# Performance work log

Measured on AMD Instinct MI355X. Metric: run time of the kernel, lower is better.

Reference implementation:

```python
import jax, jax.numpy as jnp
import numpy as np

B, D, U = 4096, 2048, 2048

def setup_inputs() -> dict:
    key = jax.random.key(0)
    ks = jax.random.split(key, 16)
    s_in = 1.0 / np.sqrt(D)
    s_h = 1.0 / np.sqrt(U)
    inp = {
        "x": jax.random.normal(ks[0], (B, D), jnp.float32),
        "h": jax.random.normal(ks[1], (B, U), jnp.float32),
        "c": jax.random.normal(ks[2], (B, U), jnp.float32),
        # input-to-gate weights (Dense with bias)
        "Wxf": jax.random.normal(ks[3], (D, U), jnp.float32) * s_in,
        "Wxi": jax.random.normal(ks[4], (D, U), jnp.float32) * s_in,
        "Wxo": jax.random.normal(ks[5], (D, U), jnp.float32) * s_in,
        "Wxg": jax.random.normal(ks[6], (D, U), jnp.float32) * s_in,
        "bf": jnp.zeros((U,), jnp.float32),
        "bi": jnp.zeros((U,), jnp.float32),
        "bo": jnp.zeros((U,), jnp.float32),
        "bg": jnp.zeros((U,), jnp.float32),
        # hidden-to-gate weights (no bias)
        "Whf": jax.random.normal(ks[7], (U, U), jnp.float32) * s_h,
        "Whi": jax.random.normal(ks[8], (U, U), jnp.float32) * s_h,
        "Who": jax.random.normal(ks[9], (U, U), jnp.float32) * s_h,
        "Whg": jax.random.normal(ks[10], (U, U), jnp.float32) * s_h,
    }
    return inp

def reference(x, h, c, Wxf, Wxi, Wxo, Wxg, bf, bi, bo, bg, Whf, Whi, Who, Whg):
    # Fuse the 8 small GEMMs into two batched GEMMs over concatenated weights,
    # then one elementwise gate-fusion pass. Math identical to per-Dense form.
    Wx = jnp.concatenate([Wxf, Wxi, Wxo, Wxg], axis=1)   # [D, 4U]
    Wh = jnp.concatenate([Whf, Whi, Who, Whg], axis=1)   # [U, 4U]
    b = jnp.concatenate([bf, bi, bo, bg], axis=0)        # [4U]
    z = x @ Wx + h @ Wh + b                               # [B, 4U]
    zf, zi, zo, zg = jnp.split(z, 4, axis=1)
    f = jax.nn.sigmoid(zf)
    i = jax.nn.sigmoid(zi)
    o = jax.nn.sigmoid(zo)
    g = jnp.tanh(zg)
    c_new = f * c + i * g
    h_new = o * jnp.tanh(c_new)
    return (h_new, c_new)
```

## Files before the change

### kernel.cpp

```cpp
#include <hip/hip_runtime.h>
#include <hip/hip_bf16.h>
#include <stdint.h>

#define B_ 4096
#define D_ 2048
#define U_ 2048
#define K_ 4096
#define N_ 8192

typedef __bf16 bf16x8 __attribute__((ext_vector_type(8)));
typedef float floatx4 __attribute__((ext_vector_type(4)));
typedef unsigned short ushort8 __attribute__((ext_vector_type(8)));

__device__ __forceinline__ unsigned short f2bf(float f) {
    union { float f; unsigned int u; } v; v.f = f;
    unsigned int u = v.u;
    unsigned int r = (u + 0x7fffu + ((u >> 16) & 1u)) >> 16;
    return (unsigned short)r;
}

__device__ __forceinline__ float bf2f(unsigned short b) {
    union { unsigned int u; float f; } v;
    v.u = ((unsigned int)b) << 16;
    return v.f;
}

__device__ __forceinline__ float sigmoid_(float x) {
    return 1.0f / (1.0f + __expf(-x));
}
__device__ __forceinline__ float tanh_(float x) {
    return 1.0f - 2.0f / (__expf(2.0f * x) + 1.0f);
}

__global__ void k_convA(const float* __restrict__ x, const float* __restrict__ h,
                        unsigned short* __restrict__ Abf) {
    int t = blockIdx.x * blockDim.x + threadIdx.x;
    long e = (long)t * 4;
    int b = (int)(e >> 12);
    int k = (int)(e & 4095);
    const float* src = (k < D_) ? (x + (size_t)b * D_ + k)
                                : (h + (size_t)b * U_ + (k - D_));
    float4 v = *(const float4*)src;
    ushort4 o;
    o.x = f2bf(v.x); o.y = f2bf(v.y); o.z = f2bf(v.z); o.w = f2bf(v.w);
    *(ushort4*)(Abf + e) = o;
}

__global__ __launch_bounds__(256) void k_convB(
        const float* __restrict__ Wx0, const float* __restrict__ Wx1,
        const float* __restrict__ Wx2, const float* __restrict__ Wx3,
        const float* __restrict__ Wh0, const float* __restrict__ Wh1,
        const float* __restrict__ Wh2, const float* __restrict__ Wh3,
        unsigned short* __restrict__ Bt) {
    __shared__ float tile[64][65];
    const int g  = blockIdx.z;
    const int k0 = blockIdx.x * 64;
    const int u0 = blockIdx.y * 64;
    const int t  = threadIdx.x;
    const float* W;
    if (k0 < D_) {
        W = (g == 0 ? Wx0 : g == 1 ? Wx1 : g == 2 ? Wx2 : Wx3) + (size_t)k0 * U_;
    } else {
        W = (g == 0 ? Wh0 : g == 1 ? Wh1 : g == 2 ? Wh2 : Wh3) + (size_t)(k0 - D_) * U_;
    }
    {
        const int kr_b = t >> 4;
        const int uc   = (t & 15) * 4;
        #pragma unroll
        for (int p = 0; p < 4; ++p) {
            int kr = p * 16 + kr_b;
            float4 v = *(const float4*)(W + (size_t)kr * U_ + u0 + uc);
            tile[kr][uc + 0] = v.x;
            tile[kr][uc + 1] = v.y;
            tile[kr][uc + 2] = v.z;
            tile[kr][uc + 3] = v.w;
        }
    }
    __syncthreads();
    {
        const int kc = (t & 7) * 8;
        #pragma unroll
        for (int p = 0; p < 2; ++p) {
            int u_idx = p * 32 + (t >> 3);
            int u = u0 + u_idx;
            int nrow = g * U_ + u;
            ushort8 o;
            #pragma unroll
            for (int kk = 0; kk < 8; ++kk)
                o[kk] = f2bf(tile[kc + kk][u_idx]);
            *(ushort8*)(Bt + (size_t)nrow * K_ + k0 + kc) = o;
        }
    }
}

__device__ __forceinline__ void gload16(const unsigned short* g, unsigned short* l) {
    __builtin_amdgcn_global_load_lds(
        (const __attribute__((address_space(1))) void*)g,
        (__attribute__((address_space(3))) void*)l, 16, 0, 0);
}

__global__ __launch_bounds__(256) void k_gemm(const unsigned short* __restrict__ A,
                                              const unsigned short* __restrict__ Bt,
                                              unsigned short* __restrict__ Z) {
    const int id    = blockIdx.x;
    const int xcd   = id & 7;
    const int s     = id >> 3;
    const int m_blk = (xcd << 2) | (s & 3);
    const int n_blk = s >> 2;
    const int m0 = m_blk * 128;
    const int n0 = n_blk * 128;

    __shared__ __align__(16) unsigned short As[2][128 * 32];
    __shared__ __align__(16) unsigned short Bs[2][128 * 32];
    const int tid = threadIdx.x;
    const int w   = tid >> 6;
    const int l   = tid & 63;

    const unsigned short* gA = A  + (size_t)(m0 + w * 16 + (l >> 2)) * K_ + (l & 3) * 8;
    const unsigned short* gB = Bt + (size_t)(n0 + w * 16 + (l >> 2)) * K_ + (l & 3) * 8;
    unsigned short* lA0 = As[0] + w * 512;
    unsigned short* lA1 = As[1] + w * 512;
    unsigned short* lB0 = Bs[0] + w * 512;
    unsigned short* lB1 = Bs[1] + w * 512;

    const int r     = l & 15;
    const int quad  = l >> 4;
    const int m_off = (w & 1) * 64;
    const int n_off = (w >> 1) * 64;

    floatx4 acc[4][4];
    #pragma unroll
    for (int i = 0; i < 4; ++i)
        #pragma unroll
        for (int j = 0; j < 4; ++j)
            #pragma unroll
            for (int e = 0; e < 4; ++e) acc[i][j][e] = 0.f;

    for (int k0 = 0; k0 < K_; k0 += 64) {
        __syncthreads();
        gload16(gA + k0,                        lA0);
        gload16(gA + k0 + (size_t)64 * K_,      lA0 + 2048);
        gload16(gB + k0,                        lB0);
        gload16(gB + k0 + (size_t)64 * K_,      lB0 + 2048);
        gload16(gA + k0 + 32,                   lA1);
        gload16(gA + k0 + 32 + (size_t)64 * K_, lA1 + 2048);
        gload16(gB + k0 + 32,                   lB1);
        gload16(gB + k0 + 32 + (size_t)64 * K_, lB1 + 2048);
        __syncthreads();

        #pragma unroll
        for (int p = 0; p < 2; ++p) {
            bf16x8 af[4], bfv[4];
            #pragma unroll
            for (int i = 0; i < 4; ++i)
                af[i] = *(const bf16x8*)(As[p] + ((m_off + i * 16 + r) * 32 + quad * 8));
            #pragma unroll
            for (int j = 0; j < 4; ++j)
                bfv[j] = *(const bf16x8*)(Bs[p] + ((n_off + j * 16 + r) * 32 + quad * 8));
            #pragma unroll
            for (int i = 0; i < 4; ++i)
                #pragma unroll
                for (int j = 0; j < 4; ++j)
                    acc[i][j] = __builtin_amdgcn_mfma_f32_16x16x32_bf16(
                        af[i], bfv[j], acc[i][j], 0, 0, 0);
        }
    }

    #pragma unroll
    for (int i = 0; i < 4; ++i) {
        #pragma unroll
        for (int j = 0; j < 4; ++j) {
            int col = n0 + n_off + j * 16 + r;
            #pragma unroll
            for (int e = 0; e < 4; ++e) {
                int row = m0 + m_off + i * 16 + quad * 4 + e;
                Z[(size_t)row * N_ + col] = f2bf(acc[i][j][e]);
            }
        }
    }
}

__global__ void k_gates(const unsigned short* __restrict__ Z, const float* __restrict__ c,
                        const float* __restrict__ bfp, const float* __restrict__ bip,
                        const float* __restrict__ bop, const float* __restrict__ bgp,
                        float* __restrict__ hout, float* __restrict__ cout) {
    int t = blockIdx.x * blockDim.x + threadIdx.x;
    long e = (long)t * 4;
    int b = (int)(e >> 11);
    int u = (int)(e & 2047);
    const size_t zr = (size_t)b * N_;
    ushort4 zf4 = *(const ushort4*)(Z + zr + u);
    ushort4 zi4 = *(const ushort4*)(Z + zr + U_ + u);
    ushort4 zo4 = *(const ushort4*)(Z + zr + 2 * U_ + u);
    ushort4 zg4 = *(const ushort4*)(Z + zr + 3 * U_ + u);
    float4 bfv = *(const float4*)(bfp + u);
    float4 biv = *(const float4*)(bip + u);
    float4 bov = *(const float4*)(bop + u);
    float4 bgv = *(const float4*)(bgp + u);
    float4 cv  = *(const float4*)(c + e);

    float zf[4] = {bf2f(zf4.x), bf2f(zf4.y), bf2f(zf4.z), bf2f(zf4.w)};
    float zi[4] = {bf2f(zi4.x), bf2f(zi4.y), bf2f(zi4.z), bf2f(zi4.w)};
    float zo[4] = {bf2f(zo4.x), bf2f(zo4.y), bf2f(zo4.z), bf2f(zo4.w)};
    float zg[4] = {bf2f(zg4.x), bf2f(zg4.y), bf2f(zg4.z), bf2f(zg4.w)};
    float bff[4] = {bfv.x, bfv.y, bfv.z, bfv.w};
    float bif[4] = {biv.x, biv.y, biv.z, biv.w};
    float bof[4] = {bov.x, bov.y, bov.z, bov.w};
    float bgf[4] = {bgv.x, bgv.y, bgv.z, bgv.w};
    float cf[4]  = {cv.x, cv.y, cv.z, cv.w};

    float hh[4], cc[4];
    #pragma unroll
    for (int q = 0; q < 4; ++q) {
        float f = sigmoid_(zf[q] + bff[q]);
        float i = sigmoid_(zi[q] + bif[q]);
        float o = sigmoid_(zo[q] + bof[q]);
        float g = tanh_(zg[q] + bgf[q]);
        float cn = f * cf[q] + i * g;
        cc[q] = cn;
        hh[q] = o * tanh_(cn);
    }
    float4 ho, co;
    ho.x = hh[0]; ho.y = hh[1]; ho.z = hh[2]; ho.w = hh[3];
    co.x = cc[0]; co.y = cc[1]; co.z = cc[2]; co.w = cc[3];
    *(float4*)(hout + e) = ho;
    *(float4*)(cout + e) = co;
}

extern "C" void kernel_launch(void* const* d_in, const int* in_sizes, int n_in,
                              void* d_out, int out_size, void* d_ws, size_t ws_size,
                              hipStream_t stream) {
    const float* x   = (const float*)d_in[0];
    const float* h   = (const float*)d_in[1];
    const float* c   = (const float*)d_in[2];
    const float* Wxf = (const float*)d_in[3];
    const float* Wxi = (const float*)d_in[4];
    const float* Wxo = (const float*)d_in[5];
    const float* Wxg = (const float*)d_in[6];
    const float* bf  = (const float*)d_in[7];
    const float* bi  = (const float*)d_in[8];
    const float* bo  = (const float*)d_in[9];
    const float* bg  = (const float*)d_in[10];
    const float* Whf = (const float*)d_in[11];
    const float* Whi = (const float*)d_in[12];
    const float* Who = (const float*)d_in[13];
    const float* Whg = (const float*)d_in[14];
    float* out = (float*)d_out;

    unsigned short* Abf = (unsigned short*)d_ws;
    unsigned short* Bt  = Abf + (size_t)B_ * K_;
    unsigned short* Z   = Bt + (size_t)N_ * K_;

    k_convA<<<(B_ * K_ / 4) / 256, 256, 0, stream>>>(x, h, Abf);
    k_convB<<<dim3(K_ / 64, U_ / 64, 4), 256, 0, stream>>>(
        Wxf, Wxi, Wxo, Wxg, Whf, Whi, Who, Whg, Bt);
    k_gemm<<<dim3((B_ / 128) * (N_ / 128)), 256, 0, stream>>>(Abf, Bt, Z);
    k_gates<<<(B_ * U_ / 4) / 256, 256, 0, stream>>>(
        Z, c, bf, bi, bo, bg, out, out + (size_t)B_ * U_);
}
```

Baseline: 553.1 us.

## Rewrite GEMM with 256x256 tiles, triple-buffered LDS, swizzled layout and staged loads

The bf16 GEMM now uses 512-thread blocks computing 256x256 tiles. K steps are 32 wide and LDS is triple-buffered, so global-to-LDS loads for step t+2 are issued between the MFMA phases of step t. An XOR swizzle on the LDS layout is meant to cut bank conflicts, and s_setprio marks the MFMA sections as high priority. This raises data reuse per block and hides load latency. In exchange it needs 96KB of LDS and many more accumulator registers, which may limit occupancy.

```diff
diff --git a/kernel.cpp b/kernel.cpp
--- a/kernel.cpp
+++ b/kernel.cpp
@@ -99,81 +99,110 @@
         (__attribute__((address_space(3))) void*)l, 16, 0, 0);
 }
 
-__global__ __launch_bounds__(256) void k_gemm(const unsigned short* __restrict__ A,
-                                              const unsigned short* __restrict__ Bt,
-                                              unsigned short* __restrict__ Z) {
-    const int id    = blockIdx.x;
-    const int xcd   = id & 7;
-    const int s     = id >> 3;
-    const int m_blk = (xcd << 2) | (s & 3);
-    const int n_blk = s >> 2;
-    const int m0 = m_blk * 128;
-    const int n0 = n_blk * 128;
-
-    __shared__ __align__(16) unsigned short As[2][128 * 32];
-    __shared__ __align__(16) unsigned short Bs[2][128 * 32];
-    const int tid = threadIdx.x;
-    const int w   = tid >> 6;
-    const int l   = tid & 63;
-
-    const unsigned short* gA = A  + (size_t)(m0 + w * 16 + (l >> 2)) * K_ + (l & 3) * 8;
-    const unsigned short* gB = Bt + (size_t)(n0 + w * 16 + (l >> 2)) * K_ + (l & 3) * 8;
-    unsigned short* lA0 = As[0] + w * 512;
-    unsigned short* lA1 = As[1] + w * 512;
-    unsigned short* lB0 = Bs[0] + w * 512;
-    unsigned short* lB1 = Bs[1] + w * 512;
-
-    const int r     = l & 15;
-    const int quad  = l >> 4;
-    const int m_off = (w & 1) * 64;
-    const int n_off = (w >> 1) * 64;
-
-    floatx4 acc[4][4];
-    #pragma unroll
-    for (int i = 0; i < 4; ++i)
+#define BARRIER() __builtin_amdgcn_s_barrier()
+
+__global__ __launch_bounds__(512, 2) void k_gemm(const unsigned short* __restrict__ A,
+                                                 const unsigned short* __restrict__ Bt,
+                                                 unsigned short* __restrict__ Z) {
+    __shared__ __align__(16) unsigned short sm[3 * 16384];
+
+    const int id  = blockIdx.x;
+    const int swz = (id & 7) * 64 + (id >> 3);
+    const int m0  = (swz & 15) << 8;
+    const int n0  = (swz >> 4) << 8;
+
+    const int tid  = threadIdx.x;
+    const int w    = tid >> 6;
+    const int l    = tid & 63;
+    const int wr   = w >> 2;
+    const int wc   = w & 3;
+    const int r    = l & 15;
+    const int quad = l >> 4;
+    const int sw8  = (quad ^ ((r >> 1) & 3)) << 3;
+
+    const int aBase = (wr * 128 + r) * 32 + sw8;
+    const int bBase = 8192 + (wc * 64 + r) * 32 + sw8;
+
+    const int srow = tid >> 2;
+    const int sg   = (((tid & 3) ^ ((srow >> 1) & 3)) << 3);
+    const unsigned short* gA0 = A  + (size_t)(m0 + srow      ) * K_ + sg;
+    const unsigned short* gA1 = A  + (size_t)(m0 + 128 + srow) * K_ + sg;
+    const unsigned short* gB0 = Bt + (size_t)(n0 + srow      ) * K_ + sg;
+    const unsigned short* gB1 = Bt + (size_t)(n0 + 128 + srow) * K_ + sg;
+    unsigned short* const stw = sm + w * 512;
+
+    floatx4 acc[8][4];
+    #pragma unroll
+    for (int i = 0; i < 8; ++i)
         #pragma unroll
         for (int j = 0; j < 4; ++j)
             #pragma unroll
             for (int e = 0; e < 4; ++e) acc[i][j][e] = 0.f;
 
-    for (int k0 = 0; k0 < K_; k0 += 64) {
-        __syncthreads();
-        gload16(gA + k0,                        lA0);
-        gload16(gA + k0 + (size_t)64 * K_,      lA0 + 2048);
-        gload16(gB + k0,                        lB0);
-        gload16(gB + k0 + (size_t)64 * K_,      lB0 + 2048);
-        gload16(gA + k0 + 32,                   lA1);
-        gload16(gA + k0 + 32 + (size_t)64 * K_, lA1 + 2048);
-        gload16(gB + k0 + 32,                   lB1);
-        gload16(gB + k0 + 32 + (size_t)64 * K_, lB1 + 2048);
-        __syncthreads();
-
-        #pragma unroll
-        for (int p = 0; p < 2; ++p) {
-            bf16x8 af[4], bfv[4];
-            #pragma unroll
-            for (int i = 0; i < 4; ++i)
-                af[i] = *(const bf16x8*)(As[p] + ((m_off + i * 16 + r) * 32 + quad * 8));
+    #pragma unroll
+    for (int tt = 0; tt < 2; ++tt) {
+        unsigned short* b = stw + tt * 16384;
+        const int kt = tt * 32;
+        gload16(gA0 + kt, b);
+        gload16(gA1 + kt, b + 4096);
+        gload16(gB0 + kt, b + 8192);
+        gload16(gB1 + kt, b + 12288);
+    }
+    asm volatile("s_waitcnt vmcnt(4)" ::: "memory");
+    BARRIER();
+
+    int c = 0;
+    for (int t = 0; t < 128; ++t) {
+        const unsigned short* Sb = sm + c * 16384;
+        const int cst = (c == 0) ? 2 : c - 1;
+        unsigned short* sb = stw + cst * 16384;
+        const int kt = (t + 2) * 32;
+        const bool st = (t < 126);
+
+        bf16x8 bq[4], aq[4];
+        #pragma unroll
+        for (int j = 0; j < 4; ++j) bq[j] = *(const bf16x8*)(Sb + bBase + j * 512);
+        #pragma unroll
+        for (int i = 0; i < 4; ++i) aq[i] = *(const bf16x8*)(Sb + aBase + i * 512);
+        if (st) { gload16(gA0 + kt, sb); gload16(gA1 + kt, sb + 4096); }
+        BARRIER();
+        __builtin_amdgcn_s_setprio(1);
+        #pragma unroll
+        for (int i = 0; i < 4; ++i)
             #pragma unroll
             for (int j = 0; j < 4; ++j)
-                bfv[j] = *(const bf16x8*)(Bs[p] + ((n_off + j * 16 + r) * 32 + quad * 8));
-            #pragma unroll
-            for (int i = 0; i < 4; ++i)
-                #pragma unroll
-                for (int j = 0; j < 4; ++j)
-                    acc[i][j] = __builtin_amdgcn_mfma_f32_16x16x32_bf16(
-                        af[i], bfv[j], acc[i][j], 0, 0, 0);
-        }
-    }
-
-    #pragma unroll
-    for (int i = 0; i < 4; ++i) {
+                acc[i][j] = __builtin_amdgcn_mfma_f32_16x16x32_bf16(
+                    aq[i], bq[j], acc[i][j], 0, 0, 0);
+        __builtin_amdgcn_s_setprio(0);
+        BARRIER();
+
+        #pragma unroll
+        for (int i = 0; i < 4; ++i) aq[i] = *(const bf16x8*)(Sb + aBase + (i + 4) * 512);
+        if (st) { gload16(gB0 + kt, sb + 8192); gload16(gB1 + kt, sb + 12288); }
+        BARRIER();
+        __builtin_amdgcn_s_setprio(1);
+        #pragma unroll
+        for (int i = 0; i < 4; ++i)
+            #pragma unroll
+            for (int j = 0; j < 4; ++j)
+                acc[i + 4][j] = __builtin_amdgcn_mfma_f32_16x16x32_bf16(
+                    aq[i], bq[j], acc[i + 4][j], 0, 0, 0);
+        __builtin_amdgcn_s_setprio(0);
+        if (st) asm volatile("s_waitcnt vmcnt(4)" ::: "memory");
+        else    asm volatile("s_waitcnt vmcnt(0)" ::: "memory");
+        BARRIER();
+
+        c = (c == 2) ? 0 : c + 1;
+    }
+
+    #pragma unroll
+    for (int i = 0; i < 8; ++i) {
         #pragma unroll
         for (int j = 0; j < 4; ++j) {
-            int col = n0 + n_off + j * 16 + r;
+            const int col = n0 + wc * 64 + j * 16 + r;
             #pragma unroll
             for (int e = 0; e < 4; ++e) {
-                int row = m0 + m_off + i * 16 + quad * 4 + e;
+                const int row = m0 + wr * 128 + i * 16 + quad * 4 + e;
                 Z[(size_t)row * N_ + col] = f2bf(acc[i][j][e]);
             }
         }
@@ -254,7 +283,7 @@
     k_convA<<<(B_ * K_ / 4) / 256, 256, 0, stream>>>(x, h, Abf);
     k_convB<<<dim3(K_ / 64, U_ / 64, 4), 256, 0, stream>>>(
         Wxf, Wxi, Wxo, Wxg, Whf, Whi, Who, Whg, Bt);
-    k_gemm<<<dim3((B_ / 128) * (N_ / 128)), 256, 0, stream>>>(Abf, Bt, Z);
+    k_gemm<<<dim3((B_ / 256) * (N_ / 256)), 512, 0, stream>>>(Abf, Bt, Z);
     k_gates<<<(B_ * U_ / 4) / 256, 256, 0, stream>>>(
         Z, c, bf, bi, bo, bg, out, out + (size_t)B_ * U_);
 }
```

Result: faster. 521.9 us (-5.6%).
